# Performance work log

Hardware: AMD Instinct MI355X
Metric: run time of the kernel (lower is better)

Reference implementation:

```python
import jax, jax.numpy as jnp
import numpy as np

B, NW, H, K = 64, 256, 768, 4
K1, Bp, AVDL = 0.1, 1.2, 50.0
ALPHA = 1.0 / H  # 1 / interaction_rep_size
BETA = 0.1


def setup_inputs() -> dict:
    key = jax.random.key(0)
    k1, k2, k3, k4, k5, k6 = jax.random.split(key, 6)
    return {
        "q_rep": jax.random.normal(k1, (B, NW, H), dtype=jnp.float32),
        "d_rep": jax.random.normal(k2, (B, NW, H), dtype=jnp.float32),
        "qtw": jax.random.uniform(k3, (B, NW), dtype=jnp.float32),
        "q_input_ids": jax.random.randint(k4, (B, NW, K), 0, 32, dtype=jnp.int32),
        "d_input_ids": jax.random.randint(k5, (B, NW, K), 0, 32, dtype=jnp.int32),
        "d_tfs": jax.random.randint(k6, (B, NW), 0, 10, dtype=jnp.int32),
    }


def _null_mask(input_ids):
    # [B, NW, 1] float mask: 0 where the whole window is zero ids
    all_zero = jnp.all(input_ids == 0, axis=2)
    return (~all_zero).astype(jnp.float32)[:, :, None]


def reference(q_rep, d_rep, qtw, q_input_ids, d_input_ids, d_tfs):
    q = q_rep * _null_mask(q_input_ids)
    d = d_rep * _null_mask(d_input_ids)

    # term-overlap scores: [B, NW, NW]
    d_expanded_tf = jnp.einsum("bqh,bdh->bqd", q, d)

    # exact match between q windows and d windows: [B, NW, NW]
    em_f = jnp.all(q_input_ids[:, :, None, :] == d_input_ids[:, None, :, :],
                   axis=3).astype(jnp.float32)

    # blended expanded term frequency, weighted by doc term frequencies
    d_tf = d_expanded_tf * (ALPHA * BETA) + em_f * (1.0 - BETA)
    tf_mult = d_tfs.astype(jnp.float32)[:, None, :]          # [B, 1, NW]
    expanded_term_df = jnp.sum(d_tf * tf_mult, axis=2)       # [B, NW]

    # BM25-like scoring
    dl = jnp.sum(d_tfs.astype(jnp.float32), axis=1, keepdims=True)  # [B, 1]
    denom = expanded_term_df * (1.0 + K1)
    nom = expanded_term_df + K1 * (1.0 - Bp + Bp * dl / AVDL)
    dtw = denom / (nom + 1e-8)
    s = jnp.sum(qtw * dtw, axis=1)                           # [B]
    return s, d_expanded_tf
```

## Files before the change

### kernel.cpp

```cpp
#include <hip/hip_runtime.h>
#include <hip/hip_bf16.h>

#define B_   64
#define NW_  256
#define H_   768

#define AB_    (0.1f / 768.0f)
#define OMB_   0.9f
#define K1_    0.1f
#define BP_    1.2f
#define AVDL_  50.0f

typedef __bf16 bf16x4 __attribute__((ext_vector_type(4)));
typedef __bf16 bf16x8 __attribute__((ext_vector_type(8)));
typedef float  f32x4  __attribute__((ext_vector_type(4)));

#define BAR_LGKM() asm volatile("s_waitcnt lgkmcnt(0)\n\ts_barrier" ::: "memory")

__global__ __launch_bounds__(256, 4) void gemm_fused(
    const float* __restrict__ q_rep, const float* __restrict__ d_rep,
    const int* __restrict__ q_ids, const int* __restrict__ d_ids,
    const int* __restrict__ d_tfs,
    float* __restrict__ S, float* __restrict__ ws_etdf)
{
    __shared__ __align__(16) __bf16 As[2][64][40];
    __shared__ __align__(16) __bf16 Bs[2][64][40];
    __shared__ float mq_s[64];
    __shared__ float md_s[64];
    __shared__ float mdtf_s[64];
    __shared__ float tf_s[64];
    __shared__ int4  qk_s[64];
    __shared__ int4  dk_s[64];

    const int tid  = threadIdx.x;
    const int wave = tid >> 6;
    const int lane = tid & 63;
    const int bid  = blockIdx.x;
    const int b    = bid & 63;
    const int t    = bid >> 6;
    const int m0   = (t & 3) * 64;
    const int n0   = (t >> 2) * 64;

    if (tid < 64) {
        int4 qa = *(const int4*)(q_ids + ((size_t)b * NW_ + m0 + tid) * 4);
        qk_s[tid] = qa;
        mq_s[tid] = (qa.x == 0 && qa.y == 0 && qa.z == 0 && qa.w == 0) ? 0.f : 1.f;
    } else if (tid < 128) {
        const int r = tid - 64;
        int4 da = *(const int4*)(d_ids + ((size_t)b * NW_ + n0 + r) * 4);
        dk_s[r] = da;
        float md = (da.x == 0 && da.y == 0 && da.z == 0 && da.w == 0) ? 0.f : 1.f;
        float tf = (float)d_tfs[(size_t)b * NW_ + n0 + r];
        md_s[r]   = md;
        tf_s[r]   = tf;
        mdtf_s[r] = md * tf;
    }

    const int srow = tid >> 3;
    const int sseg = tid & 7;
    const float* Abase = q_rep + ((size_t)b * NW_ + m0) * H_;
    const float* Bbase = d_rep + ((size_t)b * NW_ + n0) * H_;

    float4 ra0[2], rb0[2], ra1[2], rb1[2];

    auto loadg = [&](float4 (&ra)[2], float4 (&rb)[2], int kc) {
#pragma unroll
        for (int i = 0; i < 2; ++i) {
            ra[i] = *(const float4*)(Abase + (size_t)(i * 32 + srow) * H_
                                     + kc * 32 + sseg * 4);
            rb[i] = *(const float4*)(Bbase + (size_t)(i * 32 + srow) * H_
                                     + kc * 32 + sseg * 4);
        }
    };
    auto stage = [&](float4 (&ra)[2], float4 (&rb)[2], int buf) {
#pragma unroll
        for (int i = 0; i < 2; ++i) {
            bf16x4 va = { (__bf16)ra[i].x, (__bf16)ra[i].y,
                          (__bf16)ra[i].z, (__bf16)ra[i].w };
            *(bf16x4*)&As[buf][i * 32 + srow][sseg * 4] = va;
            bf16x4 vb = { (__bf16)rb[i].x, (__bf16)rb[i].y,
                          (__bf16)rb[i].z, (__bf16)rb[i].w };
            *(bf16x4*)&Bs[buf][i * 32 + srow][sseg * 4] = vb;
        }
    };

    f32x4 acc[2][2];
#pragma unroll
    for (int i = 0; i < 2; ++i)
#pragma unroll
        for (int j = 0; j < 2; ++j)
            acc[i][j] = (f32x4){0.f, 0.f, 0.f, 0.f};

    const int fr = lane & 15;
    const int fk = (lane >> 4) * 8;
    const int qm = wave >> 1;
    const int qn = wave & 1;

    loadg(ra0, rb0, 0);
    loadg(ra1, rb1, 1);
    stage(ra0, rb0, 0);
    BAR_LGKM();

#pragma unroll
    for (int kc = 0; kc < 24; ++kc) {
        const int buf = kc & 1;
        if (kc < 22) {
            if ((kc & 1) == 0) loadg(ra0, rb0, kc + 2);
            else               loadg(ra1, rb1, kc + 2);
        }
        bf16x8 af[2], bfr[2];
#pragma unroll
        for (int t2 = 0; t2 < 2; ++t2) {
            af[t2]  = *(bf16x8*)&As[buf][qm * 32 + t2 * 16 + fr][fk];
            bfr[t2] = *(bf16x8*)&Bs[buf][qn * 32 + t2 * 16 + fr][fk];
        }
#pragma unroll
        for (int i = 0; i < 2; ++i)
#pragma unroll
            for (int j = 0; j < 2; ++j)
                acc[i][j] = __builtin_amdgcn_mfma_f32_16x16x32_bf16(
                    af[i], bfr[j], acc[i][j], 0, 0, 0);
        if (kc < 23) {
            const int nb = buf ^ 1;
            if (((kc + 1) & 1) == 0) stage(ra0, rb0, nb);
            else                     stage(ra1, rb1, nb);
        }
        BAR_LGKM();
    }

    const int cn = lane & 15;
    const int qg = lane >> 4;
    float md_l[2], mdtf_l[2], tf_l[2];
    int4  dk_l[2];
#pragma unroll
    for (int j = 0; j < 2; ++j) {
        const int c = qn * 32 + j * 16 + cn;
        md_l[j]   = md_s[c];
        mdtf_l[j] = mdtf_s[c];
        tf_l[j]   = tf_s[c];
        dk_l[j]   = dk_s[c];
    }
    float* Sbase = S + ((size_t)b * NW_ + m0 + qm * 32) * NW_ + n0 + qn * 32;

    float rs[8];
#pragma unroll
    for (int i = 0; i < 2; ++i)
#pragma unroll
        for (int r = 0; r < 4; ++r) {
            const int row = i * 16 + qg * 4 + r;
            const float mq = mq_s[qm * 32 + row];
            const int4  qk = qk_s[qm * 32 + row];
            float sdot = 0.f, sem = 0.f;
#pragma unroll
            for (int j = 0; j < 2; ++j) {
                const float v = acc[i][j][r];
                Sbase[(size_t)row * NW_ + j * 16 + cn] = v * mq * md_l[j];
                sdot += v * mdtf_l[j];
                const int4 dk = dk_l[j];
                if (dk.x == qk.x && dk.y == qk.y && dk.z == qk.z && dk.w == qk.w)
                    sem += tf_l[j];
            }
            rs[i * 4 + r] = mq * AB_ * sdot + OMB_ * sem;
        }
#pragma unroll
    for (int off = 1; off <= 8; off <<= 1)
#pragma unroll
        for (int e = 0; e < 8; ++e)
            rs[e] += __shfl_xor(rs[e], off);
    if (cn == 0) {
#pragma unroll
        for (int i = 0; i < 2; ++i)
#pragma unroll
            for (int r = 0; r < 4; ++r)
                atomicAdd(&ws_etdf[(size_t)b * NW_ + m0 + qm * 32 + i * 16 + qg * 4 + r],
                          rs[i * 4 + r]);
    }
}

__global__ __launch_bounds__(64) void final_kernel(
    const float* __restrict__ ws_etdf, const int* __restrict__ d_tfs,
    const float* __restrict__ qtw, float* __restrict__ out)
{
    const int b = blockIdx.x;
    const int lane = threadIdx.x;

    float4 ev = *(const float4*)(ws_etdf + (size_t)b * NW_ + lane * 4);
    int4  tf4 = *(const int4*)(d_tfs   + (size_t)b * NW_ + lane * 4);
    float4 qv = *(const float4*)(qtw    + (size_t)b * NW_ + lane * 4);

    float dl = (float)(tf4.x + tf4.y + tf4.z + tf4.w);
#pragma unroll
    for (int off = 32; off; off >>= 1) dl += __shfl_xor(dl, off);

    const float c = K1_ * (1.f - BP_ + BP_ * dl / AVDL_);
    float ew[4] = {ev.x, ev.y, ev.z, ev.w};
    float qw[4] = {qv.x, qv.y, qv.z, qv.w};
    float s = 0.f;
#pragma unroll
    for (int j = 0; j < 4; ++j)
        s += qw[j] * (ew[j] * (1.f + K1_)) / (ew[j] + c + 1e-8f);
#pragma unroll
    for (int off = 32; off; off >>= 1) s += __shfl_xor(s, off);
    if (lane == 0) out[b] = s;
}

extern "C" void kernel_launch(void* const* d_in, const int* in_sizes, int n_in,
                              void* d_out, int out_size, void* d_ws, size_t ws_size,
                              hipStream_t stream)
{
    const float* q_rep = (const float*)d_in[0];
    const float* d_rep = (const float*)d_in[1];
    const float* qtw   = (const float*)d_in[2];
    const int*   q_ids = (const int*)d_in[3];
    const int*   d_ids = (const int*)d_in[4];
    const int*   d_tfs = (const int*)d_in[5];

    float* out = (float*)d_out;
    float* S   = out + B_;
    float* ws_etdf = (float*)d_ws;

    hipMemsetAsync(ws_etdf, 0, (size_t)B_ * NW_ * sizeof(float), stream);

    gemm_fused<<<1024, 256, 0, stream>>>(q_rep, d_rep, q_ids, d_ids, d_tfs,
                                         S, ws_etdf);
    final_kernel<<<B_, 64, 0, stream>>>(ws_etdf, d_tfs, qtw, out);
}
```

Measured before the change: 151.8 us.

## Stage 256-wide K chunks per wave with 32-deep register prefetch

Result: no change. 152.8 us (+0.7%).

```diff
diff --git a/kernel.cpp b/kernel.cpp
--- a/kernel.cpp
+++ b/kernel.cpp
@@ -15,16 +15,13 @@
 typedef __bf16 bf16x8 __attribute__((ext_vector_type(8)));
 typedef float  f32x4  __attribute__((ext_vector_type(4)));
 
-#define BAR_LGKM() asm volatile("s_waitcnt lgkmcnt(0)\n\ts_barrier" ::: "memory")
-
-__global__ __launch_bounds__(256, 4) void gemm_fused(
+__global__ __launch_bounds__(256, 2) void gemm_fused(
     const float* __restrict__ q_rep, const float* __restrict__ d_rep,
     const int* __restrict__ q_ids, const int* __restrict__ d_ids,
     const int* __restrict__ d_tfs,
     float* __restrict__ S, float* __restrict__ ws_etdf)
 {
-    __shared__ __align__(16) __bf16 As[2][64][40];
-    __shared__ __align__(16) __bf16 Bs[2][64][40];
+    __shared__ __align__(16) __bf16 Cs[128][264];
     __shared__ float mq_s[64];
     __shared__ float md_s[64];
     __shared__ float mdtf_s[64];
@@ -56,31 +53,24 @@
         mdtf_s[r] = md * tf;
     }
 
-    const int srow = tid >> 3;
-    const int sseg = tid & 7;
-    const float* Abase = q_rep + ((size_t)b * NW_ + m0) * H_;
-    const float* Bbase = d_rep + ((size_t)b * NW_ + n0) * H_;
-
-    float4 ra0[2], rb0[2], ra1[2], rb1[2];
-
-    auto loadg = [&](float4 (&ra)[2], float4 (&rb)[2], int kc) {
-#pragma unroll
-        for (int i = 0; i < 2; ++i) {
-            ra[i] = *(const float4*)(Abase + (size_t)(i * 32 + srow) * H_
-                                     + kc * 32 + sseg * 4);
-            rb[i] = *(const float4*)(Bbase + (size_t)(i * 32 + srow) * H_
-                                     + kc * 32 + sseg * 4);
-        }
+    const float* gbase = (wave < 2)
+        ? q_rep + ((size_t)b * NW_ + m0 + wave * 32) * H_
+        : d_rep + ((size_t)b * NW_ + n0 + (wave - 2) * 32) * H_;
+    const float* gl = gbase + lane * 4;
+    __bf16* lbase = &Cs[wave * 32][0] + lane * 4;
+
+    float4 rr[32];
+    auto ldall = [&](int ko) {
+#pragma unroll
+        for (int i = 0; i < 32; ++i)
+            rr[i] = *(const float4*)(gl + (size_t)i * H_ + ko * 256);
     };
-    auto stage = [&](float4 (&ra)[2], float4 (&rb)[2], int buf) {
-#pragma unroll
-        for (int i = 0; i < 2; ++i) {
-            bf16x4 va = { (__bf16)ra[i].x, (__bf16)ra[i].y,
-                          (__bf16)ra[i].z, (__bf16)ra[i].w };
-            *(bf16x4*)&As[buf][i * 32 + srow][sseg * 4] = va;
-            bf16x4 vb = { (__bf16)rb[i].x, (__bf16)rb[i].y,
-                          (__bf16)rb[i].z, (__bf16)rb[i].w };
-            *(bf16x4*)&Bs[buf][i * 32 + srow][sseg * 4] = vb;
+    auto stall = [&]() {
+#pragma unroll
+        for (int i = 0; i < 32; ++i) {
+            bf16x4 v = { (__bf16)rr[i].x, (__bf16)rr[i].y,
+                         (__bf16)rr[i].z, (__bf16)rr[i].w };
+            *(bf16x4*)(lbase + i * 264) = v;
         }
     };
 
@@ -96,36 +86,33 @@
     const int qm = wave >> 1;
     const int qn = wave & 1;
 
-    loadg(ra0, rb0, 0);
-    loadg(ra1, rb1, 1);
-    stage(ra0, rb0, 0);
-    BAR_LGKM();
-
-#pragma unroll
-    for (int kc = 0; kc < 24; ++kc) {
-        const int buf = kc & 1;
-        if (kc < 22) {
-            if ((kc & 1) == 0) loadg(ra0, rb0, kc + 2);
-            else               loadg(ra1, rb1, kc + 2);
-        }
-        bf16x8 af[2], bfr[2];
-#pragma unroll
-        for (int t2 = 0; t2 < 2; ++t2) {
-            af[t2]  = *(bf16x8*)&As[buf][qm * 32 + t2 * 16 + fr][fk];
-            bfr[t2] = *(bf16x8*)&Bs[buf][qn * 32 + t2 * 16 + fr][fk];
-        }
-#pragma unroll
-        for (int i = 0; i < 2; ++i)
-#pragma unroll
-            for (int j = 0; j < 2; ++j)
-                acc[i][j] = __builtin_amdgcn_mfma_f32_16x16x32_bf16(
-                    af[i], bfr[j], acc[i][j], 0, 0, 0);
-        if (kc < 23) {
-            const int nb = buf ^ 1;
-            if (((kc + 1) & 1) == 0) stage(ra0, rb0, nb);
-            else                     stage(ra1, rb1, nb);
-        }
-        BAR_LGKM();
+    ldall(0);
+    stall();
+    __syncthreads();
+
+#pragma unroll
+    for (int ko = 0; ko < 3; ++ko) {
+        if (ko < 2) ldall(ko + 1);
+#pragma unroll
+        for (int ks = 0; ks < 8; ++ks) {
+            bf16x8 af[2], bfr[2];
+#pragma unroll
+            for (int t2 = 0; t2 < 2; ++t2) {
+                af[t2]  = *(bf16x8*)&Cs[qm * 32 + t2 * 16 + fr][ks * 32 + fk];
+                bfr[t2] = *(bf16x8*)&Cs[64 + qn * 32 + t2 * 16 + fr][ks * 32 + fk];
+            }
+#pragma unroll
+            for (int i = 0; i < 2; ++i)
+#pragma unroll
+                for (int j = 0; j < 2; ++j)
+                    acc[i][j] = __builtin_amdgcn_mfma_f32_16x16x32_bf16(
+                        af[i], bfr[j], acc[i][j], 0, 0, 0);
+        }
+        __syncthreads();
+        if (ko < 2) {
+            stall();
+            __syncthreads();
+        }
     }
 
     const int cn = lane & 15;
```
